# Performance work log

Measured on AMD Instinct MI355X. Metric: run time of the kernel, lower is better.

## Reference

```python
import jax, jax.numpy as jnp
import numpy as np

D_MODEL = 512
D_INNER = 1024   # 2 * d_model (Mamba default expand=2)
D_STATE = 16
D_CONV = 4
DT_RANK = 32     # ceil(d_model / 16)
N_LAYERS = 2
EPS = 1e-5


def rmsnorm(x, w):
    return x * jax.lax.rsqrt(jnp.mean(x * x, axis=-1, keepdims=True) + EPS) * w


def silu(x):
    return x * jax.nn.sigmoid(x)


def causal_conv1d(x, w, b):
    # x: [B,S,di], w: [di,d_conv] depthwise, b: [di]; causal left padding
    xt = jnp.transpose(x, (0, 2, 1))                 # [B,di,S]
    k = w[:, None, :]                                # [di,1,k]
    y = jax.lax.conv_general_dilated(
        xt, k, (1,), [(D_CONV - 1, 0)],
        dimension_numbers=('NCH', 'OIH', 'NCH'),
        feature_group_count=D_INNER)
    return jnp.transpose(y, (0, 2, 1)) + b


def selective_scan(u, dt, A, Bm, C, Dp):
    # u,dt: [B,S,di]; Bm,C: [B,S,ds]; A: [di,ds]; Dp: [di]
    def step(h, inp):
        dt_t, B_t, C_t, u_t = inp                    # [B,di],[B,ds],[B,ds],[B,di]
        dA = jnp.exp(dt_t[:, :, None] * A)           # [B,di,ds]
        h = dA * h + (dt_t * u_t)[:, :, None] * B_t[:, None, :]
        y = jnp.einsum('bds,bs->bd', h, C_t)
        return h, y

    B, S, di = u.shape
    h0 = jnp.zeros((B, di, D_STATE), u.dtype)
    xs = (jnp.swapaxes(dt, 0, 1), jnp.swapaxes(Bm, 0, 1),
          jnp.swapaxes(C, 0, 1), jnp.swapaxes(u, 0, 1))
    _, ys = jax.lax.scan(step, h0, xs)               # ys: [S,B,di]
    return jnp.swapaxes(ys, 0, 1) + u * Dp


def mamba_block(x, in_proj, conv_w, conv_b, xproj, dtproj, dtproj_b, A_log, Dp, outproj):
    xz = x @ in_proj.T                               # [B,S,2*di]
    u, z = jnp.split(xz, 2, axis=-1)
    u = silu(causal_conv1d(u, conv_w, conv_b))
    x_dbl = u @ xproj.T                              # [B,S,dt_rank+2*ds]
    dt = jax.nn.softplus(x_dbl[..., :DT_RANK] @ dtproj.T + dtproj_b)
    Bm = x_dbl[..., DT_RANK:DT_RANK + D_STATE]
    C = x_dbl[..., DT_RANK + D_STATE:]
    A = -jnp.exp(A_log)
    y = selective_scan(u, dt, A, Bm, C, Dp)
    return (y * silu(z)) @ outproj.T


def setup_inputs() -> dict:
    key = jax.random.key(0)
    ks = jax.random.split(key, 8)
    B, S, L = 2, 2048, N_LAYERS

    def w(k, shape, s=0.02):
        return jax.random.normal(k, shape, jnp.float32) * s

    inp = {}
    inp['input_data'] = jax.random.normal(ks[0], (B, D_MODEL, S), jnp.float32)
    inp['mask'] = jnp.ones((B, S), jnp.bool_)
    inp['in_proj_w'] = w(ks[1], (L, 2 * D_INNER, D_MODEL))
    inp['conv_w'] = w(ks[2], (L, D_INNER, D_CONV), 0.2)
    inp['conv_b'] = jnp.zeros((L, D_INNER), jnp.float32)
    inp['xproj_w'] = w(ks[3], (L, DT_RANK + 2 * D_STATE, D_INNER))
    inp['dtproj_w'] = w(ks[4], (L, D_INNER, DT_RANK), 0.1)
    inp['dtproj_b'] = w(ks[5], (L, D_INNER), 0.5) - 4.0  # softplus -> small dt
    inp['A_log'] = jnp.log(jnp.broadcast_to(
        jnp.arange(1, D_STATE + 1, dtype=jnp.float32), (L, D_INNER, D_STATE)))
    inp['Dp'] = jnp.ones((L, D_INNER), jnp.float32)
    inp['outproj_w'] = w(ks[6], (L, D_MODEL, D_INNER))
    inp['norm_w'] = jnp.ones((L, D_MODEL), jnp.float32)
    inp['final_norm_w'] = jnp.ones((D_MODEL,), jnp.float32)
    return inp


def reference(input_data, mask, in_proj_w, conv_w, conv_b, xproj_w, dtproj_w,
              dtproj_b, A_log, Dp, outproj_w, norm_w, final_norm_w):
    x = jnp.transpose(input_data, (0, 2, 1))         # [B,S,D]
    for l in range(N_LAYERS):
        x = x + mamba_block(rmsnorm(x, norm_w[l]), in_proj_w[l], conv_w[l],
                            conv_b[l], xproj_w[l], dtproj_w[l], dtproj_b[l],
                            A_log[l], Dp[l], outproj_w[l])
    tokens = rmsnorm(x, final_norm_w)                # [B,S,D] (lm_head=Identity)
    lengths = jnp.sum(mask.astype(jnp.int32), axis=1)
    idx = jnp.maximum(lengths - 1, 0)
    emb = jnp.take_along_axis(tokens, idx[:, None, None], axis=1)[:, 0]  # [B,D]
    return tokens, emb
```

## Files before the change

### kernel.cpp

```cpp
#include <hip/hip_runtime.h>
#include <hip/hip_bf16.h>
#include <cmath>

#define BQ 2
#define SQ 2048
#define DM 512
#define DI 1024
#define DSTATE 16
#define DCONV 4
#define DTR 32
#define NLAYERS 2
#define CHUNK 32
#define NCH (SQ / CHUNK)
#define LOG2E 1.4426950408889634f

typedef __attribute__((ext_vector_type(8))) short bf16x8;
typedef __attribute__((ext_vector_type(4))) float f32x4;

__device__ __forceinline__ unsigned short f2bf(float f) {
    __hip_bfloat16 h = __float2bfloat16(f);
    return *reinterpret_cast<unsigned short*>(&h);
}

__global__ __launch_bounds__(256) void k_transpose(const float* __restrict__ in,
                                                   float* __restrict__ out) {
    __shared__ float tile[32][33];
    int b = blockIdx.z;
    int s0 = blockIdx.x * 32, c0 = blockIdx.y * 32;
    int tx = threadIdx.x, ty = threadIdx.y;
#pragma unroll
    for (int i = 0; i < 4; i++)
        tile[ty + i * 8][tx] = in[((size_t)b * DM + c0 + ty + i * 8) * SQ + s0 + tx];
    __syncthreads();
#pragma unroll
    for (int i = 0; i < 4; i++)
        out[((size_t)b * SQ + s0 + ty + i * 8) * DM + c0 + tx] = tile[tx][ty + i * 8];
}

#define N4_IN  (NLAYERS * 2 * DI * DM / 4)
#define N4_OUT (NLAYERS * DM * DI / 4)
#define N4_X   (NLAYERS * 64 * DI / 4)
#define N4_DT  (NLAYERS * DI * DTR / 4)
#define N4_ALL (N4_IN + N4_OUT + N4_X + N4_DT)

__global__ __launch_bounds__(256) void k_cvt_all(const float* __restrict__ s0,
                                                 const float* __restrict__ s1,
                                                 const float* __restrict__ s2,
                                                 const float* __restrict__ s3,
                                                 unsigned short* __restrict__ d0,
                                                 unsigned short* __restrict__ d1,
                                                 unsigned short* __restrict__ d2,
                                                 unsigned short* __restrict__ d3) {
    int i = blockIdx.x * 256 + threadIdx.x;
    if (i >= N4_ALL) return;
    const float* src; unsigned short* dst; int j = i;
    if (j < N4_IN) { src = s0; dst = d0; }
    else if ((j -= N4_IN) < N4_OUT) { src = s1; dst = d1; }
    else if ((j -= N4_OUT) < N4_X) { src = s2; dst = d2; }
    else { j -= N4_X; src = s3; dst = d3; }
    float4 v = ((const float4*)src)[j];
    ushort4 o;
    o.x = f2bf(v.x); o.y = f2bf(v.y); o.z = f2bf(v.z); o.w = f2bf(v.w);
    ((ushort4*)dst)[j] = o;
}

__global__ __launch_bounds__(256) void k_rmsnorm_bf(const float* __restrict__ x,
                                                    const float* __restrict__ w,
                                                    unsigned short* __restrict__ out) {
    int row = blockIdx.x;
    const float* xr = x + (size_t)row * DM;
    float v0 = xr[threadIdx.x];
    float v1 = xr[threadIdx.x + 256];
    float ss = v0 * v0 + v1 * v1;
#pragma unroll
    for (int off = 32; off >= 1; off >>= 1) ss += __shfl_xor(ss, off);
    __shared__ float wc[4];
    if ((threadIdx.x & 63) == 0) wc[threadIdx.x >> 6] = ss;
    __syncthreads();
    ss = wc[0] + wc[1] + wc[2] + wc[3];
    float r = rsqrtf(ss * (1.0f / DM) + 1e-5f);
    out[(size_t)row * DM + threadIdx.x] = f2bf(v0 * r * w[threadIdx.x]);
    out[(size_t)row * DM + threadIdx.x + 256] = f2bf(v1 * r * w[threadIdx.x + 256]);
}

__global__ __launch_bounds__(256) void k_rmsnorm_f32(const float* __restrict__ x,
                                                     const float* __restrict__ w,
                                                     float* __restrict__ out) {
    int row = blockIdx.x;
    const float* xr = x + (size_t)row * DM;
    float v0 = xr[threadIdx.x];
    float v1 = xr[threadIdx.x + 256];
    float ss = v0 * v0 + v1 * v1;
#pragma unroll
    for (int off = 32; off >= 1; off >>= 1) ss += __shfl_xor(ss, off);
    __shared__ float wc[4];
    if ((threadIdx.x & 63) == 0) wc[threadIdx.x >> 6] = ss;
    __syncthreads();
    ss = wc[0] + wc[1] + wc[2] + wc[3];
    float r = rsqrtf(ss * (1.0f / DM) + 1e-5f);
    out[(size_t)row * DM + threadIdx.x] = v0 * r * w[threadIdx.x];
    out[(size_t)row * DM + threadIdx.x + 256] = v1 * r * w[threadIdx.x + 256];
}

template<int BM, int BN, int AFR, int BFR>
__global__ __launch_bounds__(256) void k_gemm_bf16_t(const unsigned short* __restrict__ A, int lda,
                                                     const unsigned short* __restrict__ W, int ldw,
                                                     float* __restrict__ C, int ldc, int K,
                                                     const float* __restrict__ bias, int act,
                                                     const float* __restrict__ resid, int ldr) {
    __shared__ __align__(16) unsigned short As[BM * 32];
    __shared__ __align__(16) unsigned short Bs[BN * 32];
    const int bm = blockIdx.y * BM, bn = blockIdx.x * BN;
    const int tid = threadIdx.x;
    const int w = tid >> 6, l = tid & 63;
    const int wr = w >> 1, wc = w & 1;
    const int lg = l >> 4, lr16 = l & 15;
    f32x4 acc[AFR][BFR] = {};
    for (int k0 = 0; k0 < K; k0 += 32) {
        __syncthreads();
#pragma unroll
        for (int i = 0; i < BM / 64; i++) {
            int slot = i * 256 + tid;
            int row = slot >> 2, s = slot & 3;
            int sg = s ^ (row & 3);
            __builtin_amdgcn_global_load_lds(
                (const __attribute__((address_space(1))) unsigned int*)(A + (size_t)(bm + row) * lda + k0 + sg * 8),
                (__attribute__((address_space(3))) unsigned int*)(As + slot * 8), 16, 0, 0);
        }
#pragma unroll
        for (int i = 0; i < BN / 64; i++) {
            int slot = i * 256 + tid;
            int row = slot >> 2, s = slot & 3;
            int sg = s ^ (row & 3);
            __builtin_amdgcn_global_load_lds(
                (const __attribute__((address_space(1))) unsigned int*)(W + (size_t)(bn + row) * ldw + k0 + sg * 8),
                (__attribute__((address_space(3))) unsigned int*)(Bs + slot * 8), 16, 0, 0);
        }
        asm volatile("s_waitcnt vmcnt(0)" ::: "memory");
        __syncthreads();
        bf16x8 fa[AFR], fb[BFR];
#pragma unroll
        for (int f = 0; f < AFR; f++) {
            int ar = wr * (BM / 2) + f * 16 + lr16;
            fa[f] = *(const bf16x8*)&As[ar * 32 + (lg ^ (ar & 3)) * 8];
        }
#pragma unroll
        for (int f = 0; f < BFR; f++) {
            int br = wc * (BN / 2) + f * 16 + lr16;
            fb[f] = *(const bf16x8*)&Bs[br * 32 + (lg ^ (br & 3)) * 8];
        }
#pragma unroll
        for (int fi = 0; fi < AFR; fi++)
#pragma unroll
            for (int fj = 0; fj < BFR; fj++)
                acc[fi][fj] = __builtin_amdgcn_mfma_f32_16x16x32_bf16(fa[fi], fb[fj], acc[fi][fj], 0, 0, 0);
    }
#pragma unroll
    for (int fi = 0; fi < AFR; fi++)
#pragma unroll
        for (int fj = 0; fj < BFR; fj++)
#pragma unroll
            for (int r = 0; r < 4; r++) {
                int m = bm + wr * (BM / 2) + fi * 16 + lg * 4 + r;
                int n = bn + wc * (BN / 2) + fj * 16 + lr16;
                float v = acc[fi][fj][r];
                if (bias) v += bias[n];
                if (act == 1) v = fmaxf(v, 0.f) + log1pf(expf(-fabsf(v)));
                if (resid) v += resid[(size_t)m * ldr + n];
                C[(size_t)m * ldc + n] = v;
            }
}

__global__ __launch_bounds__(256) void k_gemm_n64_sk(const unsigned short* __restrict__ A, int lda,
                                                     const unsigned short* __restrict__ W, int ldw,
                                                     float* __restrict__ part) {
    __shared__ __align__(16) unsigned short As[128 * 32];
    __shared__ __align__(16) unsigned short Bs[64 * 32];
    const int bm = blockIdx.x * 128;
    const int koff = blockIdx.y * 128;
    const int tid = threadIdx.x;
    const int w = tid >> 6, l = tid & 63;
    const int lg = l >> 4, lr16 = l & 15;
    f32x4 acc[2][4] = {};
    for (int k0 = koff; k0 < koff + 128; k0 += 32) {
        __syncthreads();
#pragma unroll
        for (int i = 0; i < 2; i++) {
            int slot = i * 256 + tid;
            int row = slot >> 2, s = slot & 3;
            int sg = s ^ (row & 3);
            __builtin_amdgcn_global_load_lds(
                (const __attribute__((address_space(1))) unsigned int*)(A + (size_t)(bm + row) * lda + k0 + sg * 8),
                (__attribute__((address_space(3))) unsigned int*)(As + slot * 8), 16, 0, 0);
        }
        {
            int slot = tid;
            int row = slot >> 2, s = slot & 3;
            int sg = s ^ (row & 3);
            __builtin_amdgcn_global_load_lds(
                (const __attribute__((address_space(1))) unsigned int*)(W + (size_t)row * ldw + k0 + sg * 8),
                (__attribute__((address_space(3))) unsigned int*)(Bs + slot * 8), 16, 0, 0);
        }
        asm volatile("s_waitcnt vmcnt(0)" ::: "memory");
        __syncthreads();
        bf16x8 fa[2], fb[4];
#pragma unroll
        for (int f = 0; f < 2; f++) {
            int ar = w * 32 + f * 16 + lr16;
            fa[f] = *(const bf16x8*)&As[ar * 32 + (lg ^ (ar & 3)) * 8];
        }
#pragma unroll
        for (int f = 0; f < 4; f++) {
            int br = f * 16 + lr16;
            fb[f] = *(const bf16x8*)&Bs[br * 32 + (lg ^ (br & 3)) * 8];
        }
#pragma unroll
        for (int fi = 0; fi < 2; fi++)
#pragma unroll
            for (int fj = 0; fj < 4; fj++)
                acc[fi][fj] = __builtin_amdgcn_mfma_f32_16x16x32_bf16(fa[fi], fb[fj], acc[fi][fj], 0, 0, 0);
    }
    float* out = part + (size_t)blockIdx.y * ((size_t)BQ * SQ * 64);
#pragma unroll
    for (int fi = 0; fi < 2; fi++)
#pragma unroll
        for (int fj = 0; fj < 4; fj++)
#pragma unroll
            for (int r = 0; r < 4; r++) {
                int m = bm + w * 32 + fi * 16 + lg * 4 + r;
                int n = fj * 16 + lr16;
                out[(size_t)m * 64 + n] = acc[fi][fj][r];
            }
}

__global__ __launch_bounds__(256) void k_xdbl_reduce(const float* __restrict__ part,
                                                     float* __restrict__ xdbl,
                                                     unsigned short* __restrict__ xbf) {
    const int n4 = BQ * SQ * 64 / 4;
    int i = blockIdx.x * 256 + threadIdx.x;
    if (i >= n4) return;
    float4 s = ((const float4*)part)[i];
#pragma unroll
    for (int ks = 1; ks < 8; ks++) {
        float4 t = ((const float4*)part)[(size_t)ks * n4 + i];
        s.x += t.x; s.y += t.y; s.z += t.z; s.w += t.w;
    }
    ((float4*)xdbl)[i] = s;
    ushort4 o;
    o.x = f2bf(s.x); o.y = f2bf(s.y); o.z = f2bf(s.z); o.w = f2bf(s.w);
    ((ushort4*)xbf)[i] = o;
}

__global__ __launch_bounds__(256) void k_conv_silu(const float* __restrict__ xz,
                                                   const float* __restrict__ cw,
                                                   const float* __restrict__ cb,
                                                   float* __restrict__ u,
                                                   unsigned short* __restrict__ ubf) {
    int b = blockIdx.z;
    int t0 = blockIdx.x * 64;
    int d = blockIdx.y * 256 + threadIdx.x;
    float4 wv = ((const float4*)cw)[d];
    float bias = cb[d];
    const size_t rs = 2 * DI;
    size_t base = (size_t)b * SQ * rs + d;
    float x0 = 0.f, x1 = 0.f, x2 = 0.f;
    if (t0 > 0) {
        x0 = xz[base + (size_t)(t0 - 3) * rs];
        x1 = xz[base + (size_t)(t0 - 2) * rs];
        x2 = xz[base + (size_t)(t0 - 1) * rs];
    }
    for (int t = t0; t < t0 + 64; t++) {
        float x3 = xz[base + (size_t)t * rs];
        float a = bias + wv.x * x0 + wv.y * x1 + wv.z * x2 + wv.w * x3;
        float sig = 1.f / (1.f + __expf(-a));
        float v = a * sig;
        size_t o = (size_t)(b * SQ + t) * DI + d;
        u[o] = v;
        ubf[o] = f2bf(v);
        x0 = x1; x1 = x2; x2 = x3;
    }
}

__global__ __launch_bounds__(256) void k_scan_p1(const float* __restrict__ xdbl,
                                                 const float* __restrict__ dt,
                                                 const float* __restrict__ u,
                                                 const float* __restrict__ A_log,
                                                 float* __restrict__ hend,
                                                 float* __restrict__ dchunk) {
    int bc = blockIdx.x >> 4;
    int d0 = (blockIdx.x & 15) << 6;
    int b = bc >> 6;
    int c = bc & (NCH - 1);
    int tid = threadIdx.x;
    int q = tid & 3, dl = tid >> 2;
    int d = d0 + dl;
    float4 av = *(const float4*)&A_log[((size_t)d << 4) + 4 * q];
    float a0 = -expf(av.x) * LOG2E, a1 = -expf(av.y) * LOG2E;
    float a2 = -expf(av.z) * LOG2E, a3 = -expf(av.w) * LOG2E;
    float h0 = 0.f, h1 = 0.f, h2 = 0.f, h3 = 0.f, sumdt = 0.f;
    __shared__ __align__(16) float sdt[32][68], su[32][68];
    __shared__ __align__(16) float sB[32][20];
    int tbase = c * CHUNK;
#pragma unroll
    for (int i = 0; i < 2; i++) {
        int e = i * 256 + tid;
        int tt = e >> 4, j4 = e & 15;
        size_t rowm = (size_t)(b * SQ + tbase + tt);
        *(float4*)&sdt[tt][j4 * 4] = *(const float4*)&dt[rowm * DI + d0 + j4 * 4];
        *(float4*)&su[tt][j4 * 4]  = *(const float4*)&u[rowm * DI + d0 + j4 * 4];
    }
    if (tid < 128) {
        int tt = tid >> 2, j4 = tid & 3;
        size_t rowm = (size_t)(b * SQ + tbase + tt);
        *(float4*)&sB[tt][j4 * 4] = *(const float4*)&xdbl[rowm * 64 + DTR + j4 * 4];
    }
    __syncthreads();
#pragma unroll
    for (int tt = 0; tt < 32; tt++) {
        float dtv = sdt[tt][dl], uv = su[tt][dl];
        float dtu = dtv * uv;
        sumdt += dtv;
        float4 Bv = *(const float4*)&sB[tt][4 * q];
        h0 = exp2f(dtv * a0) * h0 + dtu * Bv.x;
        h1 = exp2f(dtv * a1) * h1 + dtu * Bv.y;
        h2 = exp2f(dtv * a2) * h2 + dtu * Bv.z;
        h3 = exp2f(dtv * a3) * h3 + dtu * Bv.w;
    }
    size_t o = ((size_t)bc << 14) + ((size_t)d << 4) + 4 * q;
    *(float4*)&hend[o] = make_float4(h0, h1, h2, h3);
    *(float4*)&dchunk[o] = make_float4(exp2f(a0 * sumdt), exp2f(a1 * sumdt),
                                       exp2f(a2 * sumdt), exp2f(a3 * sumdt));
}

__global__ __launch_bounds__(256) void k_scan_p2(const float* __restrict__ hend,
                                                 const float* __restrict__ dchunk,
                                                 float* __restrict__ hstart) {
    int tid = blockIdx.x * 256 + threadIdx.x;
    int b = tid >> 14;
    int ds = tid & 16383;
    float h = 0.f;
    for (int c = 0; c < NCH; c++) {
        size_t o = (((size_t)(b * NCH + c)) << 14) + ds;
        hstart[o] = h;
        h = dchunk[o] * h + hend[o];
    }
}

__global__ __launch_bounds__(256) void k_scan_p3(const float* __restrict__ xdbl,
                                                 const float* __restrict__ dt,
                                                 const float* __restrict__ u,
                                                 const float* __restrict__ xz,
                                                 const float* __restrict__ A_log,
                                                 const float* __restrict__ Dp,
                                                 const float* __restrict__ hstart,
                                                 unsigned short* __restrict__ yout) {
    int bc = blockIdx.x >> 4;
    int d0 = (blockIdx.x & 15) << 6;
    int b = bc >> 6;
    int c = bc & (NCH - 1);
    int tid = threadIdx.x;
    int q = tid & 3, dl = tid >> 2;
    int d = d0 + dl;
    int tbase = c * CHUNK;
    float zr[8];
#pragma unroll
    for (int i = 0; i < 8; i++) {
        size_t rowm = (size_t)(b * SQ + tbase + i * 4 + q);
        zr[i] = xz[rowm * (2 * DI) + DI + d];
    }
    float4 av = *(const float4*)&A_log[((size_t)d << 4) + 4 * q];
    float a0 = -expf(av.x) * LOG2E, a1 = -expf(av.y) * LOG2E;
    float a2 = -expf(av.z) * LOG2E, a3 = -expf(av.w) * LOG2E;
    size_t o = ((size_t)bc << 14) + ((size_t)d << 4) + 4 * q;
    float4 hv = *(const float4*)&hstart[o];
    float h0 = hv.x, h1 = hv.y, h2 = hv.z, h3 = hv.w;
    float Dv = Dp[d];
    __shared__ __align__(16) float sdt[32][68], su[32][68];
    __shared__ __align__(16) float sBC[32][36];
#pragma unroll
    for (int i = 0; i < 2; i++) {
        int e = i * 256 + tid;
        int tt = e >> 4, j4 = e & 15;
        size_t rowm = (size_t)(b * SQ + tbase + tt);
        *(float4*)&sdt[tt][j4 * 4] = *(const float4*)&dt[rowm * DI + d0 + j4 * 4];
        *(float4*)&su[tt][j4 * 4]  = *(const float4*)&u[rowm * DI + d0 + j4 * 4];
    }
    {
        int tt = tid >> 3, j4 = tid & 7;
        size_t rowm = (size_t)(b * SQ + tbase + tt);
        *(float4*)&sBC[tt][j4 * 4] = *(const float4*)&xdbl[rowm * 64 + DTR + j4 * 4];
    }
    __syncthreads();
#pragma unroll
    for (int tt = 0; tt < 32; tt++) {
        float dtv = sdt[tt][dl], uv = su[tt][dl];
        float dtu = dtv * uv;
        float4 Bv = *(const float4*)&sBC[tt][4 * q];
        float4 Cv = *(const float4*)&sBC[tt][16 + 4 * q];
        h0 = exp2f(dtv * a0) * h0 + dtu * Bv.x;
        h1 = exp2f(dtv * a1) * h1 + dtu * Bv.y;
        h2 = exp2f(dtv * a2) * h2 + dtu * Bv.z;
        h3 = exp2f(dtv * a3) * h3 + dtu * Bv.w;
        float y = h0 * Cv.x + h1 * Cv.y + h2 * Cv.z + h3 * Cv.w;
        y += __shfl_xor(y, 1);
        y += __shfl_xor(y, 2);
        if (q == (tt & 3)) {
            y += uv * Dv;
            float zv = zr[tt >> 2];
            float g = zv / (1.f + __expf(-zv));
            yout[(size_t)(b * SQ + tbase + tt) * DI + d] = f2bf(y * g);
        }
    }
}

__global__ __launch_bounds__(256) void k_emb(const float* __restrict__ tokens,
                                             const int* __restrict__ mask,
                                             float* __restrict__ emb) {
    int b = blockIdx.x;
    int cnt = 0;
    for (int i = threadIdx.x; i < SQ; i += 256) cnt += mask[b * SQ + i] ? 1 : 0;
#pragma unroll
    for (int off = 32; off >= 1; off >>= 1) cnt += __shfl_xor(cnt, off);
    __shared__ int wc[4];
    if ((threadIdx.x & 63) == 0) wc[threadIdx.x >> 6] = cnt;
    __syncthreads();
    int total = wc[0] + wc[1] + wc[2] + wc[3];
    int idx = total > 0 ? total - 1 : 0;
    for (int i = threadIdx.x; i < DM; i += 256)
        emb[b * DM + i] = tokens[((size_t)b * SQ + idx) * DM + i];
}

extern "C" void kernel_launch(void* const* d_in, const int* in_sizes, int n_in,
                              void* d_out, int out_size, void* d_ws, size_t ws_size,
                              hipStream_t stream) {
    const float* input_data   = (const float*)d_in[0];
    const int*   mask         = (const int*)d_in[1];
    const float* in_proj_w    = (const float*)d_in[2];
    const float* conv_w       = (const float*)d_in[3];
    const float* conv_b       = (const float*)d_in[4];
    const float* xproj_w      = (const float*)d_in[5];
    const float* dtproj_w     = (const float*)d_in[6];
    const float* dtproj_b     = (const float*)d_in[7];
    const float* A_log        = (const float*)d_in[8];
    const float* Dp           = (const float*)d_in[9];
    const float* outproj_w    = (const float*)d_in[10];
    const float* norm_w       = (const float*)d_in[11];
    const float* final_norm_w = (const float*)d_in[12];
    float* out = (float*)d_out;

    const size_t M = (size_t)BQ * SQ;
    const size_t CS = (size_t)BQ * NCH * DI * DSTATE;
    float* x              = (float*)d_ws;
    unsigned short* xn_bf = (unsigned short*)(x + M * DM);
    float* xz             = (float*)(xn_bf + M * DM);
    float* u              = xz + M * 2 * DI;
    float* xdbl           = u + M * DI;
    float* dtb            = xdbl + M * 64;
    unsigned short* ubf   = (unsigned short*)(dtb + M * DI);
    unsigned short* ybf   = ubf + M * DI;
    float* hend           = (float*)(ybf + M * DI);
    float* dchunk         = hend + CS;
    float* hstart         = dchunk + CS;
    float* xpart          = hstart + CS;
    unsigned short* xdbl_bf = (unsigned short*)(xpart + 8 * M * 64);
    unsigned short* wbf_in  = xdbl_bf + M * 64;
    unsigned short* wbf_out = wbf_in + (size_t)NLAYERS * 2 * DI * DM;
    unsigned short* wbf_x   = wbf_out + (size_t)NLAYERS * DM * DI;
    unsigned short* wbf_dt  = wbf_x + (size_t)NLAYERS * 64 * DI;

    k_cvt_all<<<(N4_ALL + 255) / 256, 256, 0, stream>>>(
        in_proj_w, outproj_w, xproj_w, dtproj_w, wbf_in, wbf_out, wbf_x, wbf_dt);

    k_transpose<<<dim3(SQ / 32, DM / 32, BQ), dim3(32, 8), 0, stream>>>(input_data, x);

    for (int l = 0; l < NLAYERS; l++) {
        k_rmsnorm_bf<<<M, 256, 0, stream>>>(x, norm_w + (size_t)l * DM, xn_bf);
        k_gemm_bf16_t<128, 128, 4, 4><<<dim3(2 * DI / 128, M / 128), 256, 0, stream>>>(
            xn_bf, DM, wbf_in + (size_t)l * 2 * DI * DM, DM, xz, 2 * DI, DM,
            nullptr, 0, nullptr, 0);
        k_conv_silu<<<dim3(SQ / 64, DI / 256, BQ), 256, 0, stream>>>(
            xz, conv_w + (size_t)l * DI * DCONV, conv_b + (size_t)l * DI, u, ubf);
        k_gemm_n64_sk<<<dim3(M / 128, 8), 256, 0, stream>>>(
            ubf, DI, wbf_x + (size_t)l * 64 * DI, DI, xpart);
        k_xdbl_reduce<<<(BQ * SQ * 64 / 4 + 255) / 256, 256, 0, stream>>>(
            xpart, xdbl, xdbl_bf);
        k_gemm_bf16_t<64, 128, 2, 4><<<dim3(DI / 128, M / 64), 256, 0, stream>>>(
            xdbl_bf, 64, wbf_dt + (size_t)l * DI * DTR, DTR, dtb, DI, DTR,
            dtproj_b + (size_t)l * DI, 1, nullptr, 0);
        k_scan_p1<<<BQ * NCH * (DI / 64), 256, 0, stream>>>(
            xdbl, dtb, u, A_log + (size_t)l * DI * DSTATE, hend, dchunk);
        k_scan_p2<<<(BQ * DI * DSTATE) / 256, 256, 0, stream>>>(hend, dchunk, hstart);
        k_scan_p3<<<BQ * NCH * (DI / 64), 256, 0, stream>>>(
            xdbl, dtb, u, xz, A_log + (size_t)l * DI * DSTATE, Dp + (size_t)l * DI,
            hstart, ybf);
        k_gemm_bf16_t<64, 128, 2, 4><<<dim3(DM / 128, M / 64), 256, 0, stream>>>(
            ybf, DI, wbf_out + (size_t)l * DM * DI, DI, x, DM, DI,
            nullptr, 0, x, DM);
    }

    k_rmsnorm_f32<<<M, 256, 0, stream>>>(x, final_norm_w, out);
    k_emb<<<BQ, 256, 0, stream>>>(out, mask, out + M * DM);
}
```

Measured before the change: 469.0 us.

## Fold inter-chunk state propagation into scan phase 3, drop p2 kernel

Removes the separate sequential inter-chunk carry kernel and has each phase-3 block recompute its starting state by walking over all preceding chunks' end states and decay factors. This saves one launch per layer and the hstart buffer write/read. In exchange it adds redundant work: chunk c re-reads c prior chunk records, so total traffic grows quadratically in the number of chunks (64) and the per-block load becomes imbalanced toward late chunks.

New measurement: 479.2 us. 1.02x slower.

```diff
diff --git a/kernel.cpp b/kernel.cpp
--- a/kernel.cpp
+++ b/kernel.cpp
@@ -332,27 +332,14 @@
                                        exp2f(a2 * sumdt), exp2f(a3 * sumdt));
 }
 
-__global__ __launch_bounds__(256) void k_scan_p2(const float* __restrict__ hend,
-                                                 const float* __restrict__ dchunk,
-                                                 float* __restrict__ hstart) {
-    int tid = blockIdx.x * 256 + threadIdx.x;
-    int b = tid >> 14;
-    int ds = tid & 16383;
-    float h = 0.f;
-    for (int c = 0; c < NCH; c++) {
-        size_t o = (((size_t)(b * NCH + c)) << 14) + ds;
-        hstart[o] = h;
-        h = dchunk[o] * h + hend[o];
-    }
-}
-
 __global__ __launch_bounds__(256) void k_scan_p3(const float* __restrict__ xdbl,
                                                  const float* __restrict__ dt,
                                                  const float* __restrict__ u,
                                                  const float* __restrict__ xz,
                                                  const float* __restrict__ A_log,
                                                  const float* __restrict__ Dp,
-                                                 const float* __restrict__ hstart,
+                                                 const float* __restrict__ hend,
+                                                 const float* __restrict__ dchunk,
                                                  unsigned short* __restrict__ yout) {
     int bc = blockIdx.x >> 4;
     int d0 = (blockIdx.x & 15) << 6;
@@ -371,9 +358,19 @@
     float4 av = *(const float4*)&A_log[((size_t)d << 4) + 4 * q];
     float a0 = -expf(av.x) * LOG2E, a1 = -expf(av.y) * LOG2E;
     float a2 = -expf(av.z) * LOG2E, a3 = -expf(av.w) * LOG2E;
-    size_t o = ((size_t)bc << 14) + ((size_t)d << 4) + 4 * q;
-    float4 hv = *(const float4*)&hstart[o];
-    float h0 = hv.x, h1 = hv.y, h2 = hv.z, h3 = hv.w;
+    float h0 = 0.f, h1 = 0.f, h2 = 0.f, h3 = 0.f;
+    {
+        size_t obase = ((size_t)d << 4) + 4 * q;
+        for (int cc = 0; cc < c; cc++) {
+            size_t o = (((size_t)(b * NCH + cc)) << 14) + obase;
+            float4 Dc = *(const float4*)&dchunk[o];
+            float4 He = *(const float4*)&hend[o];
+            h0 = Dc.x * h0 + He.x;
+            h1 = Dc.y * h1 + He.y;
+            h2 = Dc.z * h2 + He.z;
+            h3 = Dc.w * h3 + He.w;
+        }
+    }
     float Dv = Dp[d];
     __shared__ __align__(16) float sdt[32][68], su[32][68];
     __shared__ __align__(16) float sBC[32][36];
@@ -460,8 +457,7 @@
     unsigned short* ybf   = ubf + M * DI;
     float* hend           = (float*)(ybf + M * DI);
     float* dchunk         = hend + CS;
-    float* hstart         = dchunk + CS;
-    float* xpart          = hstart + CS;
+    float* xpart          = dchunk + CS;
     unsigned short* xdbl_bf = (unsigned short*)(xpart + 8 * M * 64);
     unsigned short* wbf_in  = xdbl_bf + M * 64;
     unsigned short* wbf_out = wbf_in + (size_t)NLAYERS * 2 * DI * DM;
@@ -489,10 +485,9 @@
             dtproj_b + (size_t)l * DI, 1, nullptr, 0);
         k_scan_p1<<<BQ * NCH * (DI / 64), 256, 0, stream>>>(
             xdbl, dtb, u, A_log + (size_t)l * DI * DSTATE, hend, dchunk);
-        k_scan_p2<<<(BQ * DI * DSTATE) / 256, 256, 0, stream>>>(hend, dchunk, hstart);
         k_scan_p3<<<BQ * NCH * (DI / 64), 256, 0, stream>>>(
             xdbl, dtb, u, xz, A_log + (size_t)l * DI * DSTATE, Dp + (size_t)l * DI,
-            hstart, ybf);
+            hend, dchunk, ybf);
         k_gemm_bf16_t<64, 128, 2, 4><<<dim3(DM / 128, M / 64), 256, 0, stream>>>(
             ybf, DI, wbf_out + (size_t)l * DM * DI, DI, x, DM, DI,
             nullptr, 0, x, DM);
```
